# Kernel tuning notes

Hardware: AMD Instinct MI355X
Metric: run time of the kernel (lower is better)

## Reference

```python
import jax, jax.numpy as jnp
import numpy as np

C = 128          # hidden width hard-coded in DirModelToFace
EPS = 1e-5       # BatchNorm1d eps


def sparse_bmm(rows, cols, vals, x, num_rows):
    """Batched sparse @ dense: COO (rows, cols, vals) shared across batch.
    x: [B, K, c] -> [B, num_rows, c]."""
    def one(xb):
        return jax.ops.segment_sum(xb[cols] * vals[:, None], rows, num_segments=num_rows)
    return jax.vmap(one)(x)


def conv1x1_prebn(x, gamma, beta, W, b):
    # GraphConv1x1(batch_norm='pre'): BN (training stats over B*N rows) then Linear
    mean = x.mean((0, 1))
    var = x.var((0, 1))  # biased, as torch BN uses for normalization
    xh = (x - mean) * jax.lax.rsqrt(var + EPS) * gamma + beta
    return xh @ W + b


def dir_block(Di, DiA, v, f, g, be, W, b):
    # DirResNet2 (res_f=False): quaternionic Dirac message passing
    B, N, _ = v.shape
    Fn = f.shape[1]
    msg_v = sparse_bmm(*DiA, f.reshape(B, 4 * Fn, C // 4), 4 * N).reshape(B, N, C)
    x = jax.nn.elu(jnp.concatenate([v, msg_v], axis=-1))
    v_out = v + conv1x1_prebn(x, g[0], be[0], W[0], b[0])
    msg_f = sparse_bmm(*Di, v_out.reshape(B, 4 * N, C // 4), 4 * Fn).reshape(B, Fn, C)
    x = jax.nn.elu(jnp.concatenate([f, msg_f], axis=-1))
    f_out = conv1x1_prebn(x, g[1], be[1], W[1], b[1])  # no residual on f
    return v_out, f_out


def avg_block(mask, v, g, be, W, b):
    # AvgResNet2: masked global average message
    x = v
    for j in range(2):
        x = jax.nn.elu(x)
        x_avg = (mask * x).sum(1, keepdims=True) / mask.sum(1, keepdims=True)
        x = jnp.concatenate([x, jnp.broadcast_to(x_avg, x.shape)], axis=-1)
        x = conv1x1_prebn(x, g[j], be[j], W[j], b[j])
    return x + v


def setup_inputs() -> dict:
    key = jax.random.key(0)
    ks = jax.random.split(key, 10)
    B, N, Fn = 4, 12000, 24000
    nnz = 48 * Fn  # 3 vertices per face x 4x4 quaternion block
    inputs = jax.random.normal(ks[0], (B, N, 3), jnp.float32)
    mask = jnp.ones((B, N, 1), jnp.float32)
    Di_rows = jax.random.randint(ks[1], (nnz,), 0, 4 * Fn, jnp.int32)
    Di_cols = jax.random.randint(ks[2], (nnz,), 0, 4 * N, jnp.int32)
    Di_vals = jax.random.normal(ks[3], (nnz,), jnp.float32) * 0.1
    DiA_rows = jax.random.randint(ks[4], (nnz,), 0, 4 * N, jnp.int32)
    DiA_cols = jax.random.randint(ks[5], (nnz,), 0, 4 * Fn, jnp.int32)
    DiA_vals = jax.random.normal(ks[6], (nnz,), jnp.float32) * 0.1
    W1 = jax.random.normal(ks[7], (3, C), jnp.float32) / np.sqrt(3.0)
    b1 = jnp.zeros((C,), jnp.float32)
    rn_gamma = jnp.ones((16, 2, 2 * C), jnp.float32)
    rn_beta = jnp.zeros((16, 2, 2 * C), jnp.float32)
    rn_W = jax.random.normal(ks[8], (16, 2, 2 * C, C), jnp.float32) / np.sqrt(2.0 * C)
    rn_b = jnp.zeros((16, 2, C), jnp.float32)
    g2 = jnp.ones((C,), jnp.float32)
    be2 = jnp.zeros((C,), jnp.float32)
    W2 = jax.random.normal(ks[9], (C, 1), jnp.float32) / np.sqrt(1.0 * C)
    b2 = jnp.zeros((1,), jnp.float32)
    return dict(inputs=inputs, mask=mask,
                Di_rows=Di_rows, Di_cols=Di_cols, Di_vals=Di_vals,
                DiA_rows=DiA_rows, DiA_cols=DiA_cols, DiA_vals=DiA_vals,
                W1=W1, b1=b1, rn_gamma=rn_gamma, rn_beta=rn_beta, rn_W=rn_W, rn_b=rn_b,
                g2=g2, be2=be2, W2=W2, b2=b2, num_faces=24000)


def reference(inputs, mask, Di_rows, Di_cols, Di_vals, DiA_rows, DiA_cols, DiA_vals,
              W1, b1, rn_gamma, rn_beta, rn_W, rn_b, g2, be2, W2, b2, num_faces):
    B, N, _ = inputs.shape
    v = inputs @ W1 + b1                       # conv1 (batch_norm=None)
    f = jnp.zeros((B, num_faces, C), v.dtype)  # face features start at zero
    Di = (Di_rows, Di_cols, Di_vals)
    DiA = (DiA_rows, DiA_cols, DiA_vals)
    for i in range(16):
        if i % 2 == 0:
            v, f = dir_block(Di, DiA, v, f, rn_gamma[i], rn_beta[i], rn_W[i], rn_b[i])
        else:
            v = avg_block(mask, v, rn_gamma[i], rn_beta[i], rn_W[i], rn_b[i])
    x = jax.nn.elu(f)
    return conv1x1_prebn(x, g2, be2, W2, b2)   # conv2 (batch_norm='pre')
```

## Files before the change

kernel.cpp:

```cpp
#include <hip/hip_runtime.h>
#include <hip/hip_fp16.h>
#include <math.h>


#define EPS 1e-5f

typedef float floatx4 __attribute__((ext_vector_type(4)));
typedef short shortx8 __attribute__((ext_vector_type(8)));

__device__ __forceinline__ float eluf(float x) { return x > 0.f ? x : expm1f(x); }
__device__ __forceinline__ float4 elu4(float4 v) {
    v.x = eluf(v.x); v.y = eluf(v.y); v.z = eluf(v.z); v.w = eluf(v.w); return v;
}
__device__ __forceinline__ short f2bf(float x) {
    unsigned u = __builtin_bit_cast(unsigned, x);
    u = u + 0x7FFFu + ((u >> 16) & 1u);
    return (short)(u >> 16);
}
__device__ __forceinline__ float bf2f(short h) {
    unsigned u = ((unsigned)(unsigned short)h) << 16;
    return __builtin_bit_cast(float, u);
}
__device__ __forceinline__ void split2(float x, short& hi, short& lo) {
    unsigned u = __builtin_bit_cast(unsigned, x);
    hi = (short)(u >> 16);
    float r = x - bf2f(hi);
    lo = (short)(__builtin_bit_cast(unsigned, r) >> 16);
}

__global__ void conv1_kernel(const float* __restrict__ in, const float* __restrict__ W1,
                             const float* __restrict__ b1, float* __restrict__ v,
                             __half* __restrict__ vH, int N, float* __restrict__ Sout) {
    int t = threadIdx.x;
    int c = t & 127, half = t >> 7;
    int r0 = blockIdx.x * 64;
    float w0 = W1[c], w1 = W1[128 + c], w2 = W1[256 + c], bb = b1[c];
    float s1 = 0.f, s2 = 0.f;
    for (int k = 0; k < 32; ++k) {
        int r = r0 + half + 2 * k;
        float x0 = in[r * 3 + 0], x1 = in[r * 3 + 1], x2 = in[r * 3 + 2];
        float val = bb + x0 * w0 + x1 * w1 + x2 * w2;
        v[(size_t)r * 128 + c] = val;
        int b = r / N, vert = r - b * N;
        vH[(size_t)(4 * vert + (c >> 5)) * 128 + b * 32 + (c & 31)] = __float2half(val);
        float e = eluf(val);
        s1 += e; s2 += e * e;
    }
    atomicAdd(&Sout[c], s1);
    atomicAdd(&Sout[256 + c], s2);
}

__global__ void masksum_kernel(const float* __restrict__ mask, float* __restrict__ msum,
                               int N) {
    int b = blockIdx.x, t = threadIdx.x;
    float s = 0.f;
    for (int n = t; n < N; n += 256) s += mask[(size_t)b * N + n];
    for (int o = 32; o > 0; o >>= 1) s += __shfl_down(s, o);
    __shared__ float sh[4];
    if ((t & 63) == 0) sh[t >> 6] = s;
    __syncthreads();
    if (t == 0) msum[b] = sh[0] + sh[1] + sh[2] + sh[3];
}


__global__ void hist2_kernel(const int* __restrict__ rowsA, const int* __restrict__ rowsD,
                             int* __restrict__ cntA, int* __restrict__ cntD) {
    int e = blockIdx.x * 256 + threadIdx.x;
    if (blockIdx.y == 0) atomicAdd(&cntA[rowsA[e]], 1);
    else atomicAdd(&cntD[rowsD[e]], 1);
}

__global__ void partial2_kernel(const int* __restrict__ cntA, const int* __restrict__ cntD,
                                int* __restrict__ partA, int* __restrict__ partD,
                                int RA, int RD) {
    const int* counts = blockIdx.y ? cntD : cntA;
    int* partials = blockIdx.y ? partD : partA;
    int R = blockIdx.y ? RD : RA;
    int t = threadIdx.x;
    int base = blockIdx.x * 1024 + t * 4;
    int s = 0;
#pragma unroll
    for (int j = 0; j < 4; ++j) { int i = base + j; if (i < R) s += counts[i]; }
    __shared__ int sh[256];
    sh[t] = s; __syncthreads();
    for (int st = 128; st > 0; st >>= 1) {
        if (t < st) sh[t] += sh[t + st];
        __syncthreads();
    }
    if (t == 0) partials[blockIdx.x] = sh[0];
}

__global__ void scanp2_kernel(int* __restrict__ partA, int* __restrict__ partD,
                              int* __restrict__ ptrA, int* __restrict__ ptrD,
                              int PA, int PD, int RA, int RD, int total) {
    int* partials = blockIdx.y ? partD : partA;
    int* rowptr = blockIdx.y ? ptrD : ptrA;
    int P = blockIdx.y ? PD : PA;
    int R = blockIdx.y ? RD : RA;
    __shared__ int sh[256];
    int t = threadIdx.x;
    int v = (t < P) ? partials[t] : 0;
    sh[t] = v; __syncthreads();
    for (int st = 1; st < 256; st <<= 1) {
        int tmp = (t >= st) ? sh[t - st] : 0;
        __syncthreads();
        sh[t] += tmp;
        __syncthreads();
    }
    if (t < P) partials[t] = sh[t] - v;
    if (t == 0) rowptr[R] = total;
}

__global__ void apply2_kernel(int* __restrict__ cntA, int* __restrict__ cntD,
                              const int* __restrict__ partA, const int* __restrict__ partD,
                              int* __restrict__ ptrA, int* __restrict__ ptrD,
                              int RA, int RD) {
    int* counts = blockIdx.y ? cntD : cntA;
    const int* partials = blockIdx.y ? partD : partA;
    int* rowptr = blockIdx.y ? ptrD : ptrA;
    int R = blockIdx.y ? RD : RA;
    int t = threadIdx.x;
    int base = blockIdx.x * 1024 + t * 4;
    int c[4]; int s = 0;
#pragma unroll
    for (int j = 0; j < 4; ++j) { int i = base + j; c[j] = (i < R) ? counts[i] : 0; s += c[j]; }
    __shared__ int sh[256];
    sh[t] = s; __syncthreads();
    for (int st = 1; st < 256; st <<= 1) {
        int tmp = (t >= st) ? sh[t - st] : 0;
        __syncthreads();
        sh[t] += tmp;
        __syncthreads();
    }
    int off = partials[blockIdx.x] + sh[t] - s;
#pragma unroll
    for (int j = 0; j < 4; ++j) {
        int i = base + j;
        if (i < R) { rowptr[i] = off; counts[i] = off; }
        off += c[j];
    }
}

__global__ void scatter2_kernel(const int* __restrict__ rowsA, const int* __restrict__ colsA,
                                const float* __restrict__ valsA,
                                const int* __restrict__ rowsD, const int* __restrict__ colsD,
                                const float* __restrict__ valsD,
                                int* __restrict__ fillA, int* __restrict__ fillD,
                                int2* __restrict__ edgesA, int2* __restrict__ edgesD) {
    int e = blockIdx.x * 256 + threadIdx.x;
    if (blockIdx.y == 0) {
        int p = atomicAdd(&fillA[rowsA[e]], 1);
        edgesA[p] = make_int2(colsA[e], __float_as_int(valsA[e]));
    } else {
        int p = atomicAdd(&fillD[rowsD[e]], 1);
        edgesD[p] = make_int2(colsD[e], __float_as_int(valsD[e]));
    }
}

__global__ __launch_bounds__(1024) void spmm_csr_kernel(
    const int* __restrict__ rowptr, const int2* __restrict__ edges,
    const __half2* __restrict__ xH, float* __restrict__ y, int R4,
    float* __restrict__ Sout) {
    int t = threadIdx.x;
    int waveId = blockIdx.x * 16 + (t >> 6);
    int lane = t & 63;
    int b = lane >> 4, cp = lane & 15;
    const __half2* xb = xH + b * 16 + cp;
    size_t rs = (size_t)R4 * 32;
    __shared__ float red[256];
    if (t < 256) red[t] = 0.f;
    __syncthreads();
#pragma unroll
    for (int rr = 0; rr < 2; ++rr) {
        int r = waveId * 2 + rr;
        int e0 = rowptr[r], e1 = rowptr[r + 1];
        float ax = 0.f, ay = 0.f;
        int e = e0;
        for (; e + 4 <= e1; e += 4) {
            int2 E0 = edges[e], E1 = edges[e + 1], E2 = edges[e + 2], E3 = edges[e + 3];
            __half2 g0 = xb[(size_t)E0.x * 64];
            __half2 g1 = xb[(size_t)E1.x * 64];
            __half2 g2 = xb[(size_t)E2.x * 64];
            __half2 g3 = xb[(size_t)E3.x * 64];
            float v0 = __int_as_float(E0.y), v1 = __int_as_float(E1.y);
            float v2 = __int_as_float(E2.y), v3 = __int_as_float(E3.y);
            float2 f0 = __half22float2(g0), f1 = __half22float2(g1);
            float2 f2 = __half22float2(g2), f3 = __half22float2(g3);
            ax += v0 * f0.x; ay += v0 * f0.y;
            ax += v1 * f1.x; ay += v1 * f1.y;
            ax += v2 * f2.x; ay += v2 * f2.y;
            ax += v3 * f3.x; ay += v3 * f3.y;
        }
        for (; e < e1; ++e) {
            int2 E = edges[e];
            __half2 g = xb[(size_t)E.x * 64];
            float v = __int_as_float(E.y);
            float2 f = __half22float2(g);
            ax += v * f.x; ay += v * f.y;
        }
        *(float2*)&y[(size_t)b * rs + (size_t)r * 32 + cp * 2] = make_float2(ax, ay);
        float ea = eluf(ax), eb = eluf(ay);
        float s1a = ea, s2a = ea * ea, s1b = eb, s2b = eb * eb;
        s1a += __shfl_xor(s1a, 16); s1a += __shfl_xor(s1a, 32);
        s2a += __shfl_xor(s2a, 16); s2a += __shfl_xor(s2a, 32);
        s1b += __shfl_xor(s1b, 16); s1b += __shfl_xor(s1b, 32);
        s2b += __shfl_xor(s2b, 16); s2b += __shfl_xor(s2b, 32);
        if (lane < 16) {
            int ch = (r & 3) * 32 + cp * 2;
            atomicAdd(&red[ch], s1a);
            atomicAdd(&red[ch + 1], s1b);
            atomicAdd(&red[128 + ch], s2a);
            atomicAdd(&red[128 + ch + 1], s2b);
        }
    }
    __syncthreads();
    if (t < 128) atomicAdd(&Sout[128 + t], red[t]);
    else if (t < 256) atomicAdd(&Sout[384 + (t - 128)], red[t]);
}

__global__ void fold_kernel(const float* __restrict__ S, const float* __restrict__ gamma,
                            const float* __restrict__ beta, const float* __restrict__ W,
                            const float* __restrict__ bvec, short* __restrict__ Wh,
                            short* __restrict__ Wl, float* __restrict__ bp, float invR,
                            const float* __restrict__ avgacc, const float* __restrict__ msum,
                            float* __restrict__ avgOut) {
    __shared__ float red[256];
    int o = blockIdx.x, k = threadIdx.x;
    float mean, var;
    if (avgacc != nullptr && k >= 128) {
        int c = k - 128;
        float a0 = avgacc[c] / msum[0];
        float a1 = avgacc[128 + c] / msum[1];
        float a2 = avgacc[256 + c] / msum[2];
        float a3 = avgacc[384 + c] / msum[3];
        mean = 0.25f * (a0 + a1 + a2 + a3);
        var = 0.25f * (a0 * a0 + a1 * a1 + a2 * a2 + a3 * a3) - mean * mean;
        if (o == 0) {
            avgOut[c] = a0; avgOut[128 + c] = a1;
            avgOut[256 + c] = a2; avgOut[384 + c] = a3;
        }
    } else {
        mean = S[k] * invR;
        var = S[256 + k] * invR - mean * mean;
    }
    float s = gamma[k] / sqrtf(var + EPS);
    float w = W[(size_t)k * 128 + o];
    float wp = s * w;
    short h = f2bf(wp);
    Wh[(size_t)o * 256 + k] = h;
    Wl[(size_t)o * 256 + k] = f2bf(wp - bf2f(h));
    red[k] = (beta[k] - mean * s) * w;
    __syncthreads();
    for (int st = 128; st > 0; st >>= 1) {
        if (k < st) red[k] += red[k + st];
        __syncthreads();
    }
    if (k == 0) bp[o] = bvec[o] + red[0];
}

__global__ __launch_bounds__(256) void gemm_mfma(
    const float* __restrict__ A, const float* __restrict__ Bs,
    const short* __restrict__ Wh, const short* __restrict__ Wl,
    const float* __restrict__ bp, const float* __restrict__ resid,
    float* __restrict__ out, __half* __restrict__ shadow,
    float* __restrict__ Sout, const float* __restrict__ mask,
    float* __restrict__ avgout, int rowsPerBatch, int modeB, int eluB) {
    __shared__ short Bsh[128 * 40];
    __shared__ short Bsl[128 * 40];
    const int t = threadIdx.x;
    const int lane = t & 63;
    const int wave = t >> 6;
    const int rowBase = blockIdx.x * 128 + wave * 32;
    const int m = lane & 15;
    const int kq = lane >> 4;
    floatx4 acc[2][8];
#pragma unroll
    for (int i = 0; i < 2; ++i)
#pragma unroll
        for (int j = 0; j < 8; ++j) acc[i][j] = {0.f, 0.f, 0.f, 0.f};

    const int kbEnd = (modeB == 2) ? 4 : 8;
    for (int kb = 0; kb < kbEnd; ++kb) {
        const int k0 = kb * 32 + kq * 8;
        __syncthreads();
#pragma unroll
        for (int i = 0; i < 2; ++i) {
            int idx = t + 256 * i;
            int col = idx >> 2, q = idx & 3;
            shortx8 h = *(const shortx8*)&Wh[(size_t)col * 256 + kb * 32 + q * 8];
            shortx8 l = *(const shortx8*)&Wl[(size_t)col * 256 + kb * 32 + q * 8];
            *(shortx8*)&Bsh[col * 40 + q * 8] = h;
            *(shortx8*)&Bsl[col * 40 + q * 8] = l;
        }
        shortx8 ah[2], al[2];
#pragma unroll
        for (int rg = 0; rg < 2; ++rg) {
            int row = rowBase + rg * 16 + m;
            float4 p, q;
            if (kb < 4) {
                p = elu4(*(const float4*)&A[(size_t)row * 128 + k0]);
                q = elu4(*(const float4*)&A[(size_t)row * 128 + k0 + 4]);
            } else {
                int kk = k0 - 128;
                if (modeB == 0) {
                    p = *(const float4*)&Bs[(size_t)row * 128 + kk];
                    q = *(const float4*)&Bs[(size_t)row * 128 + kk + 4];
                    if (eluB) { p = elu4(p); q = elu4(q); }
                } else {
                    int b = row / rowsPerBatch;
                    p = *(const float4*)&Bs[b * 128 + kk];
                    q = *(const float4*)&Bs[b * 128 + kk + 4];
                }
            }
            float x[8] = {p.x, p.y, p.z, p.w, q.x, q.y, q.z, q.w};
#pragma unroll
            for (int j = 0; j < 8; ++j) {
                short h, l;
                split2(x[j], h, l);
                ah[rg][j] = h;
                al[rg][j] = l;
            }
        }
        __syncthreads();
#pragma unroll
        for (int ct = 0; ct < 8; ++ct) {
            int co = (ct * 16 + m) * 40 + kq * 8;
            shortx8 bh = *(const shortx8*)&Bsh[co];
            shortx8 bl = *(const shortx8*)&Bsl[co];
#pragma unroll
            for (int rg = 0; rg < 2; ++rg) {
                acc[rg][ct] = __builtin_amdgcn_mfma_f32_16x16x32_bf16(ah[rg], bh, acc[rg][ct], 0, 0, 0);
                acc[rg][ct] = __builtin_amdgcn_mfma_f32_16x16x32_bf16(ah[rg], bl, acc[rg][ct], 0, 0, 0);
                acc[rg][ct] = __builtin_amdgcn_mfma_f32_16x16x32_bf16(al[rg], bh, acc[rg][ct], 0, 0, 0);
            }
        }
    }
    const int bBlk = (blockIdx.x * 128) / rowsPerBatch;
    float mk8[8]; int ib8[8];
    if (avgout) {
#pragma unroll
        for (int rg = 0; rg < 2; ++rg)
#pragma unroll
            for (int r = 0; r < 4; ++r) {
                int row = rowBase + rg * 16 + kq * 4 + r;
                mk8[rg * 4 + r] = mask[row];
                ib8[rg * 4 + r] = (row >= (bBlk + 1) * rowsPerBatch) ? 1 : 0;
            }
    }
    float cs1[8], cs2[8], av0[8], av1[8];
#pragma unroll
    for (int ct = 0; ct < 8; ++ct) { cs1[ct] = 0.f; cs2[ct] = 0.f; av0[ct] = 0.f; av1[ct] = 0.f; }
#pragma unroll
    for (int ct = 0; ct < 8; ++ct) {
        int col = ct * 16 + m;
        float bb = bp[col];
#pragma unroll
        for (int rg = 0; rg < 2; ++rg) {
#pragma unroll
            for (int r = 0; r < 4; ++r) {
                int row = rowBase + rg * 16 + kq * 4 + r;
                size_t o = (size_t)row * 128 + col;
                float v = acc[rg][ct][r] + bb;
                if (resid) v += resid[o];
                out[o] = v;
                if (shadow) {
                    int b = row / rowsPerBatch, vert = row - b * rowsPerBatch;
                    shadow[(size_t)(4 * vert + (col >> 5)) * 128 + b * 32 + (col & 31)] =
                        __float2half(v);
                }
                float e = eluf(v);
                cs1[ct] += e; cs2[ct] += e * e;
                if (avgout) {
                    float me = mk8[rg * 4 + r] * e;
                    if (ib8[rg * 4 + r]) av1[ct] += me; else av0[ct] += me;
                }
            }
        }
    }
    if (Sout) {
        __syncthreads();
        float* red = (float*)Bsh;
        float* redv = (float*)Bsl;
        red[t] = 0.f;
        if (avgout) redv[t] = 0.f;
        __syncthreads();
#pragma unroll
        for (int ct = 0; ct < 8; ++ct) {
            cs1[ct] += __shfl_xor(cs1[ct], 16); cs1[ct] += __shfl_xor(cs1[ct], 32);
            cs2[ct] += __shfl_xor(cs2[ct], 16); cs2[ct] += __shfl_xor(cs2[ct], 32);
            if (avgout) {
                av0[ct] += __shfl_xor(av0[ct], 16); av0[ct] += __shfl_xor(av0[ct], 32);
                av1[ct] += __shfl_xor(av1[ct], 16); av1[ct] += __shfl_xor(av1[ct], 32);
            }
        }
        if (kq == 0) {
#pragma unroll
            for (int ct = 0; ct < 8; ++ct) {
                atomicAdd(&red[ct * 16 + m], cs1[ct]);
                atomicAdd(&red[128 + ct * 16 + m], cs2[ct]);
                if (avgout) {
                    atomicAdd(&redv[ct * 16 + m], av0[ct]);
                    atomicAdd(&redv[128 + ct * 16 + m], av1[ct]);
                }
            }
        }
        __syncthreads();
        if (t < 128) atomicAdd(&Sout[t], red[t]);
        else atomicAdd(&Sout[256 + (t - 128)], red[t]);
        if (avgout) {
            int plane = t >> 7, col = t & 127;
            int b = bBlk + plane;
            if (b < 4) atomicAdd(&avgout[b * 128 + col], redv[t]);
        }
    }
}

__global__ void fold_final(const float* __restrict__ S, const float* __restrict__ g2,
                           const float* __restrict__ be2, const float* __restrict__ W2,
                           const float* __restrict__ b2, float* __restrict__ W2p, float invR) {
    __shared__ float red[128];
    int c = threadIdx.x;
    float mean = S[c] * invR;
    float var = S[256 + c] * invR - mean * mean;
    float s = g2[c] / sqrtf(var + EPS);
    float w = W2[c];
    W2p[c] = s * w;
    red[c] = (be2[c] - mean * s) * w;
    __syncthreads();
    for (int st = 64; st > 0; st >>= 1) {
        if (c < st) red[c] += red[c + st];
        __syncthreads();
    }
    if (c == 0) W2p[128] = b2[0] + red[0];
}

__global__ void final_out_kernel(const float* __restrict__ f, const float* __restrict__ W2p,
                                 float* __restrict__ out) {
    int t = threadIdx.x;
    int w = t >> 6, lane = t & 63;
    int row = blockIdx.x * 4 + w;
    float a = eluf(f[(size_t)row * 128 + lane]) * W2p[lane] +
              eluf(f[(size_t)row * 128 + 64 + lane]) * W2p[64 + lane];
    for (int off = 32; off > 0; off >>= 1) a += __shfl_down(a, off);
    if (lane == 0) out[row] = a + W2p[128];
}

extern "C" void kernel_launch(void* const* d_in, const int* in_sizes, int n_in,
                              void* d_out, int out_size, void* d_ws, size_t ws_size,
                              hipStream_t stream) {
    const float* inputs = (const float*)d_in[0];
    const float* mask = (const float*)d_in[1];
    const int* Di_rows = (const int*)d_in[2];
    const int* Di_cols = (const int*)d_in[3];
    const float* Di_vals = (const float*)d_in[4];
    const int* DiA_rows = (const int*)d_in[5];
    const int* DiA_cols = (const int*)d_in[6];
    const float* DiA_vals = (const float*)d_in[7];
    const float* W1 = (const float*)d_in[8];
    const float* b1 = (const float*)d_in[9];
    const float* rn_gamma = (const float*)d_in[10];
    const float* rn_beta = (const float*)d_in[11];
    const float* rn_W = (const float*)d_in[12];
    const float* rn_b = (const float*)d_in[13];
    const float* g2 = (const float*)d_in[14];
    const float* be2 = (const float*)d_in[15];
    const float* W2 = (const float*)d_in[16];
    const float* b2 = (const float*)d_in[17];
    float* out = (float*)d_out;

    const int B = 4;
    const int BN = in_sizes[1];
    const int N = BN / B;
    const int BF = out_size;
    const int Fn = BF / B;
    const int nnz = in_sizes[2];
    const int RA = 4 * N;
    const int RD = 4 * Fn;

    float* ws = (float*)d_ws;
    size_t off = 0;
    float* vA = ws + off;  off += (size_t)BN * 128;
    float* fA = ws + off;  off += (size_t)BF * 128;
    float* msg = ws + off; off += (size_t)BF * 128;
    __half* vH = (__half*)(ws + off); off += (size_t)RA * 128 / 2;
    __half* fH = (__half*)(ws + off); off += (size_t)RD * 128 / 2;
    int* ptrA    = (int*)(ws + off);  off += (size_t)RA + 4;
    int2* edgesA = (int2*)(ws + off); off += (size_t)nnz * 2;
    int* ptrD    = (int*)(ws + off);  off += (size_t)RD + 4;
    int2* edgesD = (int2*)(ws + off); off += (size_t)nnz * 2;
    int* cntA    = (int*)(ws + off);  off += (size_t)RA;
    int* cntD    = (int*)(ws + off);  off += (size_t)RD;
    int* partA   = (int*)(ws + off);  off += 256;
    int* partD   = (int*)(ws + off);  off += 256;
    float* Sarena = ws + off; off += 33 * 512;
    float* Aarena = ws + off; off += 16 * 512;
    float* msum = ws + off;   off += 4;
    float* avg = ws + off;    off += 512;
    short* Wh = (short*)(ws + off); off += 128 * 256 / 2;
    short* Wl = (short*)(ws + off); off += 128 * 256 / 2;
    float* bp = ws + off;  off += 128;
    float* W2p = ws + off; off += 132;

    const int eBlocks = nnz / 256;
    const int PA = (RA + 1023) / 1024;
    const int PD = (RD + 1023) / 1024;

    hipMemsetAsync(Sarena, 0, (33 * 512 + 16 * 512) * 4, stream);
    hipMemsetAsync(fA, 0, (size_t)BF * 128 * 4, stream);
    hipMemsetAsync(cntA, 0, (size_t)(RA + RD) * 4, stream);

    hist2_kernel<<<dim3(eBlocks, 2), 256, 0, stream>>>(DiA_rows, Di_rows, cntA, cntD);
    partial2_kernel<<<dim3(PD, 2), 256, 0, stream>>>(cntA, cntD, partA, partD, RA, RD);
    scanp2_kernel<<<dim3(1, 2), 256, 0, stream>>>(partA, partD, ptrA, ptrD, PA, PD,
                                                  RA, RD, nnz);
    apply2_kernel<<<dim3(PD, 2), 256, 0, stream>>>(cntA, cntD, partA, partD, ptrA, ptrD,
                                                   RA, RD);
    scatter2_kernel<<<dim3(eBlocks, 2), 256, 0, stream>>>(DiA_rows, DiA_cols, DiA_vals,
                                                          Di_rows, Di_cols, Di_vals,
                                                          cntA, cntD, edgesA, edgesD);

    auto slot = [&](int i, int j) { return Sarena + 512 * (2 * i + j); };
    float* Sfinal = Sarena + 512 * 32;

    masksum_kernel<<<B, 256, 0, stream>>>(mask, msum, N);
    conv1_kernel<<<BN / 64, 256, 0, stream>>>(inputs, W1, b1, vA, vH, N, slot(0, 0));

    for (int i = 0; i < 15; ++i) {
        if ((i & 1) == 0) {
            const float* g0 = rn_gamma + (size_t)(i * 2 + 0) * 256;
            const float* be0 = rn_beta + (size_t)(i * 2 + 0) * 256;
            const float* Wl0 = rn_W + (size_t)(i * 2 + 0) * 256 * 128;
            const float* bl0 = rn_b + (size_t)(i * 2 + 0) * 128;
            const float* g1 = rn_gamma + (size_t)(i * 2 + 1) * 256;
            const float* be1 = rn_beta + (size_t)(i * 2 + 1) * 256;
            const float* Wl1 = rn_W + (size_t)(i * 2 + 1) * 256 * 128;
            const float* bl1 = rn_b + (size_t)(i * 2 + 1) * 128;
            float* SoutV = (i < 14) ? slot(i + 1, 0) : nullptr;
            float* avgV = (i < 14) ? (Aarena + 512 * i) : nullptr;

            if (i == 0) {
                fold_kernel<<<128, 256, 0, stream>>>(slot(0, 0), g0, be0, Wl0, bl0,
                                                     Wh, Wl, bp, 1.f / BN,
                                                     nullptr, nullptr, nullptr);
                gemm_mfma<<<BN / 128, 256, 0, stream>>>(vA, nullptr, Wh, Wl, bp, vA, vA,
                                                        vH, SoutV, mask, avgV, N, 2, 1);
            } else {
                spmm_csr_kernel<<<RA / 32, 1024, 0, stream>>>(ptrA, edgesA,
                                                              (const __half2*)fH, msg, RA,
                                                              slot(i, 0));
                fold_kernel<<<128, 256, 0, stream>>>(slot(i, 0), g0, be0, Wl0, bl0,
                                                     Wh, Wl, bp, 1.f / BN,
                                                     nullptr, nullptr, nullptr);
                gemm_mfma<<<BN / 128, 256, 0, stream>>>(vA, msg, Wh, Wl, bp, vA, vA,
                                                        vH, SoutV, mask, avgV, N, 0, 1);
            }

            spmm_csr_kernel<<<RD / 32, 1024, 0, stream>>>(ptrD, edgesD, (const __half2*)vH,
                                                          msg, RD, slot(i, 1));
            fold_kernel<<<128, 256, 0, stream>>>(slot(i, 1), g1, be1, Wl1, bl1, Wh, Wl,
                                                 bp, 1.f / BF, nullptr, nullptr, nullptr);
            gemm_mfma<<<BF / 128, 256, 0, stream>>>(fA, msg, Wh, Wl, bp, nullptr, fA, fH,
                                                    (i < 14) ? slot(i + 2, 1) : Sfinal,
                                                    nullptr, nullptr, Fn, 0, 1);
        } else {
            for (int j = 0; j < 2; ++j) {
                const float* g = rn_gamma + (size_t)(i * 2 + j) * 256;
                const float* be = rn_beta + (size_t)(i * 2 + j) * 256;
                const float* Wlw = rn_W + (size_t)(i * 2 + j) * 256 * 128;
                const float* bl = rn_b + (size_t)(i * 2 + j) * 128;
                const float* src = (j == 0) ? vA : msg;
                float* dst = (j == 0) ? msg : vA;
                const float* resid = (j == 0) ? nullptr : vA;
                __half* shadow = (j == 0) ? nullptr : vH;
                float* Sout = (j == 0) ? slot(i, 1) : slot(i + 1, 0);
                float* avgO = (j == 0) ? (Aarena + 512 * i) : nullptr;

                float* avgacc = Aarena + 512 * (i - 1 + j);
                fold_kernel<<<128, 256, 0, stream>>>(slot(i, j), g, be, Wlw, bl, Wh, Wl,
                                                     bp, 1.f / BN, avgacc, msum, avg);
                gemm_mfma<<<BN / 128, 256, 0, stream>>>(src, avg, Wh, Wl, bp, resid, dst,
                                                        shadow, Sout, mask, avgO, N, 1, 0);
            }
        }
    }

    fold_final<<<1, 128, 0, stream>>>(Sfinal, g2, be2, W2, b2, W2p, 1.f / BF);
    final_out_kernel<<<BF / 4, 256, 0, stream>>>(fA, W2p, out);
}
```

Baseline: 4.157 ms.

## Fold BatchNorm weight folding into GEMM kernel and merge masksum into conv1

Result: no change. 4.155 ms (-0.0%).

```diff
diff --git a/kernel.cpp b/kernel.cpp
--- a/kernel.cpp
+++ b/kernel.cpp
@@ -30,8 +30,21 @@
 
 __global__ void conv1_kernel(const float* __restrict__ in, const float* __restrict__ W1,
                              const float* __restrict__ b1, float* __restrict__ v,
-                             __half* __restrict__ vH, int N, float* __restrict__ Sout) {
+                             __half* __restrict__ vH, int N, float* __restrict__ Sout,
+                             const float* __restrict__ mask, float* __restrict__ msum,
+                             int nConv) {
+    __shared__ float sh[4];
     int t = threadIdx.x;
+    if (blockIdx.x >= nConv) {
+        int b = blockIdx.x - nConv;
+        float s = 0.f;
+        for (int n = t; n < N; n += 256) s += mask[(size_t)b * N + n];
+        for (int o = 32; o > 0; o >>= 1) s += __shfl_down(s, o);
+        if ((t & 63) == 0) sh[t >> 6] = s;
+        __syncthreads();
+        if (t == 0) msum[b] = sh[0] + sh[1] + sh[2] + sh[3];
+        return;
+    }
     int c = t & 127, half = t >> 7;
     int r0 = blockIdx.x * 64;
     float w0 = W1[c], w1 = W1[128 + c], w2 = W1[256 + c], bb = b1[c];
@@ -48,18 +61,6 @@
     }
     atomicAdd(&Sout[c], s1);
     atomicAdd(&Sout[256 + c], s2);
-}
-
-__global__ void masksum_kernel(const float* __restrict__ mask, float* __restrict__ msum,
-                               int N) {
-    int b = blockIdx.x, t = threadIdx.x;
-    float s = 0.f;
-    for (int n = t; n < N; n += 256) s += mask[(size_t)b * N + n];
-    for (int o = 32; o > 0; o >>= 1) s += __shfl_down(s, o);
-    __shared__ float sh[4];
-    if ((t & 63) == 0) sh[t >> 6] = s;
-    __syncthreads();
-    if (t == 0) msum[b] = sh[0] + sh[1] + sh[2] + sh[3];
 }
 
 
@@ -218,67 +219,59 @@
     else if (t < 256) atomicAdd(&Sout[384 + (t - 128)], red[t]);
 }
 
-__global__ void fold_kernel(const float* __restrict__ S, const float* __restrict__ gamma,
-                            const float* __restrict__ beta, const float* __restrict__ W,
-                            const float* __restrict__ bvec, short* __restrict__ Wh,
-                            short* __restrict__ Wl, float* __restrict__ bp, float invR,
-                            const float* __restrict__ avgacc, const float* __restrict__ msum,
-                            float* __restrict__ avgOut) {
-    __shared__ float red[256];
-    int o = blockIdx.x, k = threadIdx.x;
-    float mean, var;
-    if (avgacc != nullptr && k >= 128) {
-        int c = k - 128;
-        float a0 = avgacc[c] / msum[0];
-        float a1 = avgacc[128 + c] / msum[1];
-        float a2 = avgacc[256 + c] / msum[2];
-        float a3 = avgacc[384 + c] / msum[3];
-        mean = 0.25f * (a0 + a1 + a2 + a3);
-        var = 0.25f * (a0 * a0 + a1 * a1 + a2 * a2 + a3 * a3) - mean * mean;
-        if (o == 0) {
-            avgOut[c] = a0; avgOut[128 + c] = a1;
-            avgOut[256 + c] = a2; avgOut[384 + c] = a3;
-        }
-    } else {
-        mean = S[k] * invR;
-        var = S[256 + k] * invR - mean * mean;
-    }
-    float s = gamma[k] / sqrtf(var + EPS);
-    float w = W[(size_t)k * 128 + o];
-    float wp = s * w;
-    short h = f2bf(wp);
-    Wh[(size_t)o * 256 + k] = h;
-    Wl[(size_t)o * 256 + k] = f2bf(wp - bf2f(h));
-    red[k] = (beta[k] - mean * s) * w;
-    __syncthreads();
-    for (int st = 128; st > 0; st >>= 1) {
-        if (k < st) red[k] += red[k + st];
-        __syncthreads();
-    }
-    if (k == 0) bp[o] = bvec[o] + red[0];
-}
-
 __global__ __launch_bounds__(256) void gemm_mfma(
     const float* __restrict__ A, const float* __restrict__ Bs,
-    const short* __restrict__ Wh, const short* __restrict__ Wl,
-    const float* __restrict__ bp, const float* __restrict__ resid,
+    const float* __restrict__ S, const float* __restrict__ gvec,
+    const float* __restrict__ bevec, const float* __restrict__ Wfull,
+    const float* __restrict__ bvec, const float* __restrict__ resid,
     float* __restrict__ out, __half* __restrict__ shadow,
     float* __restrict__ Sout, const float* __restrict__ mask,
-    float* __restrict__ avgout, int rowsPerBatch, int modeB, int eluB) {
+    float* __restrict__ avgout, const float* __restrict__ avgacc,
+    const float* __restrict__ msum, float invR,
+    int rowsPerBatch, int modeB, int eluB) {
     __shared__ short Bsh[128 * 40];
     __shared__ short Bsl[128 * 40];
+    __shared__ float sS[256];
+    __shared__ float sMS[256];
+    __shared__ float avgLDS[512];
+    __shared__ float bparr[256];
+    __shared__ float bpF[128];
     const int t = threadIdx.x;
     const int lane = t & 63;
     const int wave = t >> 6;
     const int rowBase = blockIdx.x * 128 + wave * 32;
     const int m = lane & 15;
     const int kq = lane >> 4;
+
+    {
+        int k = t;
+        float mean, var;
+        if (modeB == 1 && k >= 128) {
+            int c = k - 128;
+            float a0 = avgacc[c] / msum[0];
+            float a1 = avgacc[128 + c] / msum[1];
+            float a2 = avgacc[256 + c] / msum[2];
+            float a3 = avgacc[384 + c] / msum[3];
+            avgLDS[c] = a0; avgLDS[128 + c] = a1;
+            avgLDS[256 + c] = a2; avgLDS[384 + c] = a3;
+            mean = 0.25f * (a0 + a1 + a2 + a3);
+            var = 0.25f * (a0 * a0 + a1 * a1 + a2 * a2 + a3 * a3) - mean * mean;
+        } else {
+            mean = S[k] * invR;
+            var = S[256 + k] * invR - mean * mean;
+        }
+        float s = gvec[k] / sqrtf(var + EPS);
+        sS[k] = s;
+        sMS[k] = bevec[k] - mean * s;
+    }
+
     floatx4 acc[2][8];
 #pragma unroll
     for (int i = 0; i < 2; ++i)
 #pragma unroll
         for (int j = 0; j < 8; ++j) acc[i][j] = {0.f, 0.f, 0.f, 0.f};
 
+    float bpp0 = 0.f, bpp1 = 0.f;
     const int kbEnd = (modeB == 2) ? 4 : 8;
     for (int kb = 0; kb < kbEnd; ++kb) {
         const int k0 = kb * 32 + kq * 8;
@@ -286,11 +279,22 @@
 #pragma unroll
         for (int i = 0; i < 2; ++i) {
             int idx = t + 256 * i;
-            int col = idx >> 2, q = idx & 3;
-            shortx8 h = *(const shortx8*)&Wh[(size_t)col * 256 + kb * 32 + q * 8];
-            shortx8 l = *(const shortx8*)&Wl[(size_t)col * 256 + kb * 32 + q * 8];
-            *(shortx8*)&Bsh[col * 40 + q * 8] = h;
-            *(shortx8*)&Bsl[col * 40 + q * 8] = l;
+            int col = idx & 127, qs = idx >> 7;
+            shortx8 hv, lv;
+            float bps = 0.f;
+#pragma unroll
+            for (int j = 0; j < 8; ++j) {
+                int k = kb * 32 + qs * 8 + j;
+                float w = Wfull[(size_t)k * 128 + col];
+                float wp = sS[k] * w;
+                short h = f2bf(wp);
+                hv[j] = h;
+                lv[j] = f2bf(wp - bf2f(h));
+                bps += sMS[k] * w;
+            }
+            *(shortx8*)&Bsh[col * 40 + qs * 8] = hv;
+            *(shortx8*)&Bsl[col * 40 + qs * 8] = lv;
+            if (i == 0) bpp0 += bps; else bpp1 += bps;
         }
         shortx8 ah[2], al[2];
 #pragma unroll
@@ -308,8 +312,8 @@
                     if (eluB) { p = elu4(p); q = elu4(q); }
                 } else {
                     int b = row / rowsPerBatch;
-                    p = *(const float4*)&Bs[b * 128 + kk];
-                    q = *(const float4*)&Bs[b * 128 + kk + 4];
+                    p = *(const float4*)&avgLDS[b * 128 + kk];
+                    q = *(const float4*)&avgLDS[b * 128 + kk + 4];
                 }
             }
             float x[8] = {p.x, p.y, p.z, p.w, q.x, q.y, q.z, q.w};
@@ -335,6 +339,20 @@
             }
         }
     }
+    if (modeB == 2) {
+        int col = t & 127;
+        float bps = 0.f;
+        for (int j = 0; j < 64; ++j) {
+            int k = 128 + (t >> 7) * 64 + j;
+            bps += sMS[k] * Wfull[(size_t)k * 128 + col];
+        }
+        bpp0 += bps;
+    }
+    bparr[t] = bpp0 + bpp1;
+    __syncthreads();
+    if (t < 128) bpF[t] = bvec[t] + bparr[t] + bparr[t + 128];
+    __syncthreads();
+
     const int bBlk = (blockIdx.x * 128) / rowsPerBatch;
     float mk8[8]; int ib8[8];
     if (avgout) {
@@ -353,7 +371,7 @@
 #pragma unroll
     for (int ct = 0; ct < 8; ++ct) {
         int col = ct * 16 + m;
-        float bb = bp[col];
+        float bb = bpF[col];
 #pragma unroll
         for (int rg = 0; rg < 2; ++rg) {
 #pragma unroll
@@ -438,11 +456,16 @@
                                  float* __restrict__ out) {
     int t = threadIdx.x;
     int w = t >> 6, lane = t & 63;
-    int row = blockIdx.x * 4 + w;
-    float a = eluf(f[(size_t)row * 128 + lane]) * W2p[lane] +
-              eluf(f[(size_t)row * 128 + 64 + lane]) * W2p[64 + lane];
-    for (int off = 32; off > 0; off >>= 1) a += __shfl_down(a, off);
-    if (lane == 0) out[row] = a + W2p[128];
+    float wa = W2p[lane], wb = W2p[64 + lane], bb = W2p[128];
+    int base = blockIdx.x * 16 + w * 4;
+#pragma unroll
+    for (int rr = 0; rr < 4; ++rr) {
+        int row = base + rr;
+        float a = eluf(f[(size_t)row * 128 + lane]) * wa +
+                  eluf(f[(size_t)row * 128 + 64 + lane]) * wb;
+        for (int off = 32; off > 0; off >>= 1) a += __shfl_down(a, off);
+        if (lane == 0) out[row] = a + bb;
+    }
 }
 
 extern "C" void kernel_launch(void* const* d_in, const int* in_sizes, int n_in,
@@ -495,10 +518,6 @@
     float* Sarena = ws + off; off += 33 * 512;
     float* Aarena = ws + off; off += 16 * 512;
     float* msum = ws + off;   off += 4;
-    float* avg = ws + off;    off += 512;
-    short* Wh = (short*)(ws + off); off += 128 * 256 / 2;
-    short* Wl = (short*)(ws + off); off += 128 * 256 / 2;
-    float* bp = ws + off;  off += 128;
     float* W2p = ws + off; off += 132;
 
     const int eBlocks = nnz / 256;
@@ -522,8 +541,8 @@
     auto slot = [&](int i, int j) { return Sarena + 512 * (2 * i + j); };
     float* Sfinal = Sarena + 512 * 32;
 
-    masksum_kernel<<<B, 256, 0, stream>>>(mask, msum, N);
-    conv1_kernel<<<BN / 64, 256, 0, stream>>>(inputs, W1, b1, vA, vH, N, slot(0, 0));
+    conv1_kernel<<<BN / 64 + B, 256, 0, stream>>>(inputs, W1, b1, vA, vH, N, slot(0, 0),
+                                                  mask, msum, BN / 64);
 
     for (int i = 0; i < 15; ++i) {
         if ((i & 1) == 0) {
@@ -539,29 +558,27 @@
             float* avgV = (i < 14) ? (Aarena + 512 * i) : nullptr;
 
             if (i == 0) {
-                fold_kernel<<<128, 256, 0, stream>>>(slot(0, 0), g0, be0, Wl0, bl0,
-                                                     Wh, Wl, bp, 1.f / BN,
-                                                     nullptr, nullptr, nullptr);
-                gemm_mfma<<<BN / 128, 256, 0, stream>>>(vA, nullptr, Wh, Wl, bp, vA, vA,
-                                                        vH, SoutV, mask, avgV, N, 2, 1);
+                gemm_mfma<<<BN / 128, 256, 0, stream>>>(vA, nullptr, slot(0, 0), g0, be0,
+                                                        Wl0, bl0, vA, vA, vH, SoutV, mask,
+                                                        avgV, nullptr, nullptr, 1.f / BN,
+                                                        N, 2, 1);
             } else {
                 spmm_csr_kernel<<<RA / 32, 1024, 0, stream>>>(ptrA, edgesA,
                                                               (const __half2*)fH, msg, RA,
                                                               slot(i, 0));
-                fold_kernel<<<128, 256, 0, stream>>>(slot(i, 0), g0, be0, Wl0, bl0,
-                                                     Wh, Wl, bp, 1.f / BN,
-                                                     nullptr, nullptr, nullptr);
-                gemm_mfma<<<BN / 128, 256, 0, stream>>>(vA, msg, Wh, Wl, bp, vA, vA,
-                                                        vH, SoutV, mask, avgV, N, 0, 1);
+                gemm_mfma<<<BN / 128, 256, 0, stream>>>(vA, msg, slot(i, 0), g0, be0,
+                                                        Wl0, bl0, vA, vA, vH, SoutV, mask,
+                                                        avgV, nullptr, nullptr, 1.f / BN,
+                                                        N, 0, 1);
             }
 
             spmm_csr_kernel<<<RD / 32, 1024, 0, stream>>>(ptrD, edgesD, (const __half2*)vH,
                                                           msg, RD, slot(i, 1));
-            fold_kernel<<<128, 256, 0, stream>>>(slot(i, 1), g1, be1, Wl1, bl1, Wh, Wl,
-                                                 bp, 1.f / BF, nullptr, nullptr, nullptr);
-            gemm_mfma<<<BF / 128, 256, 0, stream>>>(fA, msg, Wh, Wl, bp, nullptr, fA, fH,
+            gemm_mfma<<<BF / 128, 256, 0, stream>>>(fA, msg, slot(i, 1), g1, be1, Wl1, bl1,
+                                                    nullptr, fA, fH,
                                                     (i < 14) ? slot(i + 2, 1) : Sfinal,
-                                                    nullptr, nullptr, Fn, 0, 1);
+                                                    nullptr, nullptr, nullptr, nullptr,
+                                                    1.f / BF, Fn, 0, 1);
         } else {
             for (int j = 0; j < 2; ++j) {
                 const float* g = rn_gamma + (size_t)(i * 2 + j) * 256;
@@ -572,18 +589,18 @@
                 float* dst = (j == 0) ? msg : vA;
                 const float* resid = (j == 0) ? nullptr : vA;
                 __half* shadow = (j == 0) ? nullptr : vH;
-                float* Sout = (j == 0) ? slot(i, 1) : slot(i + 1, 0);
+                float* SoutP = (j == 0) ? slot(i, 1) : slot(i + 1, 0);
                 float* avgO = (j == 0) ? (Aarena + 512 * i) : nullptr;
-
-                float* avgacc = Aarena + 512 * (i - 1 + j);
-                fold_kernel<<<128, 256, 0, stream>>>(slot(i, j), g, be, Wlw, bl, Wh, Wl,
-                                                     bp, 1.f / BN, avgacc, msum, avg);
-                gemm_mfma<<<BN / 128, 256, 0, stream>>>(src, avg, Wh, Wl, bp, resid, dst,
-                                                        shadow, Sout, mask, avgO, N, 1, 0);
+                const float* avgacc = Aarena + 512 * (i - 1 + j);
+
+                gemm_mfma<<<BN / 128, 256, 0, stream>>>(src, nullptr, slot(i, j), g, be,
+                                                        Wlw, bl, resid, dst, shadow, SoutP,
+                                                        mask, avgO, avgacc, msum,
+                                                        1.f / BN, N, 1, 0);
             }
         }
     }
 
     fold_final<<<1, 128, 0, stream>>>(Sfinal, g2, be2, W2, b2, W2p, 1.f / BF);
-    final_out_kernel<<<BF / 4, 256, 0, stream>>>(fA, W2p, out);
-}
+    final_out_kernel<<<BF / 16, 256, 0, stream>>>(fA, W2p, out);
+}
```
